# Performance work log

Hardware: AMD Instinct MI355X
Metric: run time of the kernel (lower is better)

The kernel has to match this reference:

```python
import jax, jax.numpy as jnp
import numpy as np

ETA = 1e-5  # option['eta']


def setup_inputs() -> dict:
    key = jax.random.key(0)
    k1, k2, k3, k4 = jax.random.split(key, 4)
    d, N, two_m = 1024, 20000, 512  # num_feature, num_data, 2*m
    At = jax.random.normal(k1, (d, N), dtype=jnp.float32)
    b = jax.random.normal(k2, (N,), dtype=jnp.float32)
    w1_init = jax.random.normal(k3, (d,), dtype=jnp.float32)
    W2_init = jax.random.normal(k4, (two_m, d - 1), dtype=jnp.float32)
    return {"At": At, "b": b, "w1_init": w1_init, "W2_init": W2_init}


def _ftrl_scan(At, b, w1_init, W2_init):
    # Sequential FTRL-style online FM update (task='reg'), faithful to the torch loop.
    def step(carry, xs):
        w1, W2, g_w1, g_W2 = carry
        x, bi = xs                     # x: (d,), bi: scalar
        a = x[:-1]                     # alpha[:-1], (d-1,)
        t = W2 @ a                     # (2m,) == W2.matmul(alpha[:-1])
        scalar = jnp.dot(w1, x) + jnp.dot(t, t)   # w1^T x + t^T t
        sign = 2.0 * (scalar - bi)     # grad of squared loss
        g_w1 = g_w1 + sign * x
        g_W2 = g_W2 + 2.0 * jnp.outer(t, a)       # 2 * (W2 a) a^T
        w1_new = -ETA * g_w1
        W2_new = -ETA * g_W2
        return (w1_new, W2_new, g_w1, g_W2), scalar

    carry0 = (w1_init, W2_init, jnp.zeros_like(w1_init), jnp.zeros_like(W2_init))
    _, preds = jax.lax.scan(step, carry0, (At.T, b))  # scan over num_data
    return preds


def reference(At, b, w1_init, W2_init):
    preds = _ftrl_scan(At, b, w1_init, W2_init)
    return preds, b  # (pred_list, real_list)
```

## Files before the change

### kernel.cpp

```cpp
#include <hip/hip_runtime.h>


#define NN 20000
#define CC 16
#define NCH 1250
#define ETA2 2e-5f
#define XPAD 1028

#define OFF_GRAM 0L
#define OFF_Z    150016L
#define OFF_SCLP 1430016L
#define OFF_ACC  1430080L
#define OFF_TV   1450080L
#define OFF_X0   1470080L

__global__ __launch_bounds__(1024) void k_init(
    const float* __restrict__ At, const float* __restrict__ bvec,
    const float* __restrict__ w1, const float* __restrict__ W2,
    float* __restrict__ out, float* __restrict__ scalp,
    float* __restrict__ x0ws) {
  __shared__ float x0s[1024];
  __shared__ float part[16];
  const int bid = blockIdx.x, t = threadIdx.x;
  const int wid = t >> 6, lane = t & 63;

  if (bid < 32) {
    x0s[t] = (t < 1023) ? At[(long)t * NN] : 0.f;
    __syncthreads();
    const int row = bid * 16 + wid;
    float p = 0.f;
#pragma unroll
    for (int k = 0; k < 16; ++k) {
      const int ci = k * 64 + lane;
      if (ci < 1023) p = fmaf(W2[(long)row * 1023 + ci], x0s[ci], p);
    }
#pragma unroll
    for (int o = 32; o > 0; o >>= 1) p += __shfl_down(p, o);
    if (lane == 0) part[wid] = p * p;
    __syncthreads();
    if (t == 0) {
      float s = 0.f;
#pragma unroll
      for (int k = 0; k < 16; ++k) s += part[k];
      scalp[bid] = s;
    }
  } else if (bid == 32) {
    const float xv = At[(long)t * NN];
    x0ws[t] = xv;
    float p = w1[t] * xv;
#pragma unroll
    for (int o = 32; o > 0; o >>= 1) p += __shfl_down(p, o);
    if (lane == 0) part[wid] = p;
    __syncthreads();
    if (t == 0) {
      float s = 0.f;
#pragma unroll
      for (int k = 0; k < 16; ++k) s += part[k];
      scalp[32] = s;
    }
  } else {
    const int i = (bid - 33) * 1000 + t;
    if (t < 1000) out[NN + i] = bvec[i];
  }
}

#define STAGE_LD(g, dst)                                          \
  {                                                               \
    const int e_ = (g) >> 2, q_ = (g) & 3;                        \
    dst = *(const float4*)(At + (long)e_ * NN + i0 + 4 * q_);     \
  }
#define STAGE_ST(g, src, xl)                                      \
  {                                                               \
    const int e_ = (g) >> 2, q_ = (g) & 3;                        \
    xl[(4 * q_ + 0) * XPAD + e_] = src.x;                         \
    xl[(4 * q_ + 1) * XPAD + e_] = src.y;                         \
    xl[(4 * q_ + 2) * XPAD + e_] = src.z;                         \
    xl[(4 * q_ + 3) * XPAD + e_] = src.w;                         \
  }

struct GramSh {
  __align__(16) float xl[CC * XPAD];
  __align__(16) float x0s[1024];
  float up[64];
  float rs[CC];
  float sc[2];
};
static_assert(sizeof(GramSh) <= 80 * 1024, "LDS too big for 2 blocks/CU");

#define GACC(r, s, RA, RB)                      \
  ac[r][s] = fmaf(RA.x, RB.x, ac[r][s]);        \
  ac[r][s] = fmaf(RA.y, RB.y, ac[r][s]);        \
  ac[r][s] = fmaf(RA.z, RB.z, ac[r][s]);        \
  ac[r][s] = fmaf(RA.w, RB.w, ac[r][s]);

__global__ __launch_bounds__(1024, 4) void k_gram(
    const float* __restrict__ At, const float* __restrict__ bvec,
    const float* __restrict__ x0g, float* __restrict__ gram,
    float* __restrict__ Zr, const float* __restrict__ scalp,
    float* __restrict__ acc) {
  __shared__ GramSh sh;
  const int c = blockIdx.x, t = threadIdx.x;
  const long i0 = (long)c * CC;

  sh.x0s[t] = x0g[t];
  if (t == 0) {
    float T = 0.f;
#pragma unroll
    for (int k = 0; k < 32; ++k) T += scalp[k];
    sh.sc[0] = T;
    sh.sc[1] = scalp[32];
  }

  const bool act = (t < 320);
  const int tile = t >> 5, band = t & 31;
  int a = 0, bb = 0;
  if (act) {
    int r = tile;
    while (r > a) { r -= ++a; }
    bb = r;
  }
  const bool uact = (t >= 320 && t < 384);
  const int uz = t - 320, ub = uz >> 4, ui = uz & 15;
  float4 uac = make_float4(0.f, 0.f, 0.f, 0.f);

  float ac[4][4];
#pragma unroll
  for (int r = 0; r < 4; ++r)
#pragma unroll
    for (int s = 0; s < 4; ++s) ac[r][s] = 0.f;

#define GRAM_PHASE(H)                                                        \
  if (act) {                                                                 \
    _Pragma("unroll") for (int k = 0; k < 4; ++k) {                          \
      const int e0 = (H) * 512 + (band + 32 * k) * 4;                        \
      const float4 A0 = *(const float4*)&sh.xl[(4 * a + 0) * XPAD + e0];     \
      const float4 A1 = *(const float4*)&sh.xl[(4 * a + 1) * XPAD + e0];     \
      const float4 A2 = *(const float4*)&sh.xl[(4 * a + 2) * XPAD + e0];     \
      const float4 A3 = *(const float4*)&sh.xl[(4 * a + 3) * XPAD + e0];     \
      const float4 B0 = *(const float4*)&sh.xl[(4 * bb + 0) * XPAD + e0];    \
      const float4 B1 = *(const float4*)&sh.xl[(4 * bb + 1) * XPAD + e0];    \
      const float4 B2 = *(const float4*)&sh.xl[(4 * bb + 2) * XPAD + e0];    \
      const float4 B3 = *(const float4*)&sh.xl[(4 * bb + 3) * XPAD + e0];    \
      GACC(0, 0, A0, B0) GACC(0, 1, A0, B1) GACC(0, 2, A0, B2)               \
      GACC(0, 3, A0, B3) GACC(1, 0, A1, B0) GACC(1, 1, A1, B1)               \
      GACC(1, 2, A1, B2) GACC(1, 3, A1, B3) GACC(2, 0, A2, B0)               \
      GACC(2, 1, A2, B1) GACC(2, 2, A2, B2) GACC(2, 3, A2, B3)               \
      GACC(3, 0, A3, B0) GACC(3, 1, A3, B1) GACC(3, 2, A3, B2)               \
      GACC(3, 3, A3, B3)                                                     \
    }                                                                        \
  } else if (uact) {                                                         \
    _Pragma("unroll") for (int k = 0; k < 32; ++k) {                         \
      const int e0 = (H) * 512 + ub * 128 + 4 * k;                           \
      const float4 xv = *(const float4*)&sh.xl[ui * XPAD + e0];              \
      const float4 x0 = *(const float4*)&sh.x0s[e0];                         \
      uac.x = fmaf(x0.x, xv.x, uac.x);                                       \
      uac.y = fmaf(x0.y, xv.y, uac.y);                                       \
      uac.z = fmaf(x0.z, xv.z, uac.z);                                       \
      uac.w = fmaf(x0.w, xv.w, uac.w);                                       \
    }                                                                        \
  }

  float4 ha, hb;
  STAGE_LD(t, ha);
  STAGE_LD(1024 + t, hb);
  STAGE_ST(t, ha, sh.xl);
  STAGE_ST(1024 + t, hb, sh.xl);
  __syncthreads();

  STAGE_LD(2048 + t, ha);
  STAGE_LD(3072 + t, hb);

  GRAM_PHASE(0)

  STAGE_ST(2048 + t, ha, sh.xl);
  STAGE_ST(3072 + t, hb, sh.xl);
  __syncthreads();

  GRAM_PHASE(1)

  if (act) {
#pragma unroll
    for (int off = 16; off >= 1; off >>= 1)
#pragma unroll
      for (int r = 0; r < 4; ++r)
#pragma unroll
        for (int s = 0; s < 4; ++s) ac[r][s] += __shfl_xor(ac[r][s], off);
    if (band == 0) {
      float* gp = gram + (long)c * 120;
#pragma unroll
      for (int r = 0; r < 4; ++r) {
        const int row = 4 * a + r;
        const int base = row * (row - 1) / 2;
#pragma unroll
        for (int s = 0; s < 4; ++s) {
          const int col = 4 * bb + s;
          if (col < row) gp[base + col] = ac[r][s];
        }
      }
    }
  }
  if (uact) sh.up[uz] = uac.x + uac.y + uac.z + uac.w;
  __syncthreads();

  if (t < CC) {
    const long gi = i0 + t;
    const float uu = sh.up[t] + sh.up[16 + t] + sh.up[32 + t] + sh.up[48 + t];
    const float qi = sh.xl[t * XPAD + 1023];
    const float q0 = sh.x0s[1023];
    const float al = (gi == 0) ? 1.f : -ETA2 * (uu - q0 * qi);
    const float T0 = sh.sc[0], s0v = sh.sc[1];
    const float bv = bvec[gi];
    float r = 2.f * fmaf(al * al, T0, -bv);
    if (gi == 0) r = 2.f * (s0v + T0 - bv);
    sh.rs[t] = r;
    acc[gi] = r;
  }
  __syncthreads();

  {
    float z = 0.f;
#pragma unroll
    for (int j = 0; j < CC; ++j) z = fmaf(sh.rs[j], sh.xl[j * XPAD + t], z);
    Zr[(long)c * 1024 + t] = z;
  }
}

__global__ __launch_bounds__(1024) void k_scan(float* __restrict__ Z) {
  __shared__ float gsum[32][33];
  const int t = threadIdx.x;
  const int ei = t & 31, ci = t >> 5;
  const int e = blockIdx.x * 32 + ei;
  const int c0 = ci * 40;
  const int c1 = (c0 + 40 < NCH) ? c0 + 40 : NCH;

  float s = 0.f;
  for (int base = c0; base < c1; base += 8) {
    float v[8];
#pragma unroll
    for (int k = 0; k < 8; ++k) {
      const int cc = base + k;
      v[k] = (cc < c1) ? Z[(long)cc * 1024 + e] : 0.f;
    }
#pragma unroll
    for (int k = 0; k < 8; ++k) s += v[k];
  }
  gsum[ci][ei] = s;
  __syncthreads();

  float off = 0.f;
#pragma unroll
  for (int k = 0; k < 31; ++k)
    if (k < ci) off += gsum[k][ei];

  s = off;
  for (int base = c0; base < c1; base += 8) {
    float v[8];
#pragma unroll
    for (int k = 0; k < 8; ++k) {
      const int cc = base + k;
      v[k] = (cc < c1) ? Z[(long)cc * 1024 + e] : 0.f;
    }
#pragma unroll
    for (int k = 0; k < 8; ++k) {
      const int cc = base + k;
      if (cc < c1) Z[(long)cc * 1024 + e] = s;
      s += v[k];
    }
  }
}

struct TermSh {
  __align__(16) float xl[CC * XPAD];
  __align__(16) float Sm[1024];
  float red[512];
  float vvs[CC], wvs[CC];
};
static_assert(sizeof(TermSh) <= 80 * 1024, "LDS too big for 2 blocks/CU");

template <bool LAST>
__global__ __launch_bounds__(1024, 4) void k_term(
    const float* __restrict__ At, const float* __restrict__ bvec,
    const float* __restrict__ gram, const float* __restrict__ S,
    float* __restrict__ Z1, float* __restrict__ acc, float* __restrict__ tvec,
    float* __restrict__ out) {
  __shared__ TermSh sh;
  const int c = blockIdx.x, t = threadIdx.x;
  const long i0 = (long)c * CC;

  sh.Sm[t] = S[(long)c * 1024 + t];
  if (t < CC) sh.vvs[t] = LAST ? tvec[i0 + t] : acc[i0 + t];

  const bool sact = (t < 512);
  const int si = t >> 5, sb = t & 31;
  float p = 0.f;

#define SWEEP_PHASE(H)                                            \
  if (sact) {                                                     \
    _Pragma("unroll") for (int k = 0; k < 4; ++k) {               \
      const int e0 = (H) * 512 + (sb + 32 * k) * 4;               \
      const float4 xv = *(const float4*)&sh.xl[si * XPAD + e0];   \
      const float4 sv = *(const float4*)&sh.Sm[e0];               \
      p = fmaf(xv.x, sv.x, p);                                    \
      p = fmaf(xv.y, sv.y, p);                                    \
      p = fmaf(xv.z, sv.z, p);                                    \
      p = fmaf(xv.w, sv.w, p);                                    \
    }                                                             \
  }

  float4 ha, hb;
  STAGE_LD(t, ha);
  STAGE_LD(1024 + t, hb);
  STAGE_ST(t, ha, sh.xl);
  STAGE_ST(1024 + t, hb, sh.xl);
  __syncthreads();

  STAGE_LD(2048 + t, ha);
  STAGE_LD(3072 + t, hb);

  SWEEP_PHASE(0)

  STAGE_ST(2048 + t, ha, sh.xl);
  STAGE_ST(3072 + t, hb, sh.xl);
  __syncthreads();

  SWEEP_PHASE(1)

  if (sact) sh.red[t] = p;
  __syncthreads();

  if (t < CC) {
    const int i = t;
    float dot = 0.f;
#pragma unroll
    for (int k = 0; k < 32; ++k) dot += sh.red[i * 32 + k];
    const float* grow = gram + (long)c * 120 + i * (i - 1) / 2;
    float g = 0.f;
#pragma unroll 4
    for (int j = 0; j < i; ++j) g = fmaf(grow[j], sh.vvs[j], g);
    const float w = -ETA2 * (dot + g);
    if (LAST) {
      out[i0 + i] = fmaf(0.5f, acc[i0 + i] + w, bvec[i0 + i]);
    } else {
      sh.wvs[i] = w;
      tvec[i0 + i] = w;
      acc[i0 + i] += w;
    }
  }
  if (!LAST) {
    __syncthreads();
    float z = 0.f;
#pragma unroll
    for (int j = 0; j < CC; ++j) z = fmaf(sh.wvs[j], sh.xl[j * XPAD + t], z);
    Z1[(long)c * 1024 + t] = z;
  }
}

extern "C" void kernel_launch(void* const* d_in, const int* in_sizes, int n_in,
                              void* d_out, int out_size, void* d_ws,
                              size_t ws_size, hipStream_t stream) {
  const float* At = (const float*)d_in[0];
  const float* b  = (const float*)d_in[1];
  const float* w1 = (const float*)d_in[2];
  const float* W2 = (const float*)d_in[3];
  float* out = (float*)d_out;
  float* ws = (float*)d_ws;

  float* gram  = ws + OFF_GRAM;
  float* Zsh   = ws + OFF_Z;
  float* scalp = ws + OFF_SCLP;
  float* acc   = ws + OFF_ACC;
  float* tvec  = ws + OFF_TV;
  float* x0ws  = ws + OFF_X0;

  k_init<<<dim3(53), dim3(1024), 0, stream>>>(At, b, w1, W2, out, scalp, x0ws);
  k_gram<<<dim3(NCH), dim3(1024), 0, stream>>>(At, b, x0ws, gram, Zsh, scalp,
                                               acc);
  k_scan<<<dim3(32), dim3(1024), 0, stream>>>(Zsh);
  k_term<false><<<dim3(NCH), dim3(1024), 0, stream>>>(At, b, gram, Zsh, Zsh,
                                                      acc, tvec, out);
  k_scan<<<dim3(32), dim3(1024), 0, stream>>>(Zsh);
  k_term<true><<<dim3(NCH), dim3(1024), 0, stream>>>(At, b, gram, Zsh, Zsh,
                                                     acc, tvec, out);
}
```

Baseline: 228.1 us.

## Halve chunk size and cache chunk-transposed X copy for term passes

Chunk size drops from 16 to 8 columns, so there are 2500 blocks and a smaller triangular Gram (28 entries per chunk) computed one pair per warp-group. The Gram kernel can also write a chunk-major contiguous copy of X into workspace. The term kernels then read it with coalesced float4 loads instead of strided At gathers and LDS transposes, and reduce with wave shuffles. This trades extra workspace traffic (an 80MB copy written once, read twice) against the strided loads, and doubles the length of the scan over chunks.

```diff
diff --git a/kernel.cpp b/kernel.cpp
--- a/kernel.cpp
+++ b/kernel.cpp
@@ -2,17 +2,19 @@
 
 
 #define NN 20000
-#define CC 16
-#define NCH 1250
+#define CC 8
+#define NCH 2500
 #define ETA2 2e-5f
-#define XPAD 1028
+#define XST 1032
 
 #define OFF_GRAM 0L
-#define OFF_Z    150016L
-#define OFF_SCLP 1430016L
-#define OFF_ACC  1430080L
-#define OFF_TV   1450080L
-#define OFF_X0   1470080L
+#define OFF_Z    70016L
+#define OFF_SCLP 2630016L
+#define OFF_ACC  2630080L
+#define OFF_TV   2650112L
+#define OFF_X0   2670144L
+#define OFF_XC   2671168L
+#define WS_NEED_BYTES ((size_t)(OFF_XC + 20480000L) * 4)
 
 __global__ __launch_bounds__(1024) void k_init(
     const float* __restrict__ At, const float* __restrict__ bvec,
@@ -64,40 +66,31 @@
   }
 }
 
-#define STAGE_LD(g, dst)                                          \
-  {                                                               \
-    const int e_ = (g) >> 2, q_ = (g) & 3;                        \
-    dst = *(const float4*)(At + (long)e_ * NN + i0 + 4 * q_);     \
-  }
-#define STAGE_ST(g, src, xl)                                      \
-  {                                                               \
-    const int e_ = (g) >> 2, q_ = (g) & 3;                        \
-    xl[(4 * q_ + 0) * XPAD + e_] = src.x;                         \
-    xl[(4 * q_ + 1) * XPAD + e_] = src.y;                         \
-    xl[(4 * q_ + 2) * XPAD + e_] = src.z;                         \
-    xl[(4 * q_ + 3) * XPAD + e_] = src.w;                         \
+#define STAGE8(g, xl)                                               \
+  {                                                                 \
+    const int e_ = (g) >> 1, q_ = (g) & 1;                          \
+    const float4 v_ =                                               \
+        *(const float4*)(At + (long)e_ * NN + i0 + 4 * q_);         \
+    xl[(4 * q_ + 0) * XST + e_] = v_.x;                             \
+    xl[(4 * q_ + 1) * XST + e_] = v_.y;                             \
+    xl[(4 * q_ + 2) * XST + e_] = v_.z;                             \
+    xl[(4 * q_ + 3) * XST + e_] = v_.w;                             \
   }
 
 struct GramSh {
-  __align__(16) float xl[CC * XPAD];
+  __align__(16) float xl[CC * XST];
   __align__(16) float x0s[1024];
-  float up[64];
+  float usum[CC];
   float rs[CC];
   float sc[2];
 };
-static_assert(sizeof(GramSh) <= 80 * 1024, "LDS too big for 2 blocks/CU");
-
-#define GACC(r, s, RA, RB)                      \
-  ac[r][s] = fmaf(RA.x, RB.x, ac[r][s]);        \
-  ac[r][s] = fmaf(RA.y, RB.y, ac[r][s]);        \
-  ac[r][s] = fmaf(RA.z, RB.z, ac[r][s]);        \
-  ac[r][s] = fmaf(RA.w, RB.w, ac[r][s]);
+static_assert(sizeof(GramSh) <= 64 * 1024, "LDS must stay under 64KB");
 
 __global__ __launch_bounds__(1024, 4) void k_gram(
     const float* __restrict__ At, const float* __restrict__ bvec,
     const float* __restrict__ x0g, float* __restrict__ gram,
     float* __restrict__ Zr, const float* __restrict__ scalp,
-    float* __restrict__ acc) {
+    float* __restrict__ acc, float* __restrict__ Xc, const int writeXc) {
   __shared__ GramSh sh;
   const int c = blockIdx.x, t = threadIdx.x;
   const long i0 = (long)c * CC;
@@ -111,101 +104,52 @@
     sh.sc[1] = scalp[32];
   }
 
-  const bool act = (t < 320);
-  const int tile = t >> 5, band = t & 31;
-  int a = 0, bb = 0;
-  if (act) {
-    int r = tile;
-    while (r > a) { r -= ++a; }
-    bb = r;
-  }
-  const bool uact = (t >= 320 && t < 384);
-  const int uz = t - 320, ub = uz >> 4, ui = uz & 15;
-  float4 uac = make_float4(0.f, 0.f, 0.f, 0.f);
-
-  float ac[4][4];
-#pragma unroll
-  for (int r = 0; r < 4; ++r)
-#pragma unroll
-    for (int s = 0; s < 4; ++s) ac[r][s] = 0.f;
-
-#define GRAM_PHASE(H)                                                        \
-  if (act) {                                                                 \
-    _Pragma("unroll") for (int k = 0; k < 4; ++k) {                          \
-      const int e0 = (H) * 512 + (band + 32 * k) * 4;                        \
-      const float4 A0 = *(const float4*)&sh.xl[(4 * a + 0) * XPAD + e0];     \
-      const float4 A1 = *(const float4*)&sh.xl[(4 * a + 1) * XPAD + e0];     \
-      const float4 A2 = *(const float4*)&sh.xl[(4 * a + 2) * XPAD + e0];     \
-      const float4 A3 = *(const float4*)&sh.xl[(4 * a + 3) * XPAD + e0];     \
-      const float4 B0 = *(const float4*)&sh.xl[(4 * bb + 0) * XPAD + e0];    \
-      const float4 B1 = *(const float4*)&sh.xl[(4 * bb + 1) * XPAD + e0];    \
-      const float4 B2 = *(const float4*)&sh.xl[(4 * bb + 2) * XPAD + e0];    \
-      const float4 B3 = *(const float4*)&sh.xl[(4 * bb + 3) * XPAD + e0];    \
-      GACC(0, 0, A0, B0) GACC(0, 1, A0, B1) GACC(0, 2, A0, B2)               \
-      GACC(0, 3, A0, B3) GACC(1, 0, A1, B0) GACC(1, 1, A1, B1)               \
-      GACC(1, 2, A1, B2) GACC(1, 3, A1, B3) GACC(2, 0, A2, B0)               \
-      GACC(2, 1, A2, B1) GACC(2, 2, A2, B2) GACC(2, 3, A2, B3)               \
-      GACC(3, 0, A3, B0) GACC(3, 1, A3, B1) GACC(3, 2, A3, B2)               \
-      GACC(3, 3, A3, B3)                                                     \
-    }                                                                        \
-  } else if (uact) {                                                         \
-    _Pragma("unroll") for (int k = 0; k < 32; ++k) {                         \
-      const int e0 = (H) * 512 + ub * 128 + 4 * k;                           \
-      const float4 xv = *(const float4*)&sh.xl[ui * XPAD + e0];              \
-      const float4 x0 = *(const float4*)&sh.x0s[e0];                         \
-      uac.x = fmaf(x0.x, xv.x, uac.x);                                       \
-      uac.y = fmaf(x0.y, xv.y, uac.y);                                       \
-      uac.z = fmaf(x0.z, xv.z, uac.z);                                       \
-      uac.w = fmaf(x0.w, xv.w, uac.w);                                       \
-    }                                                                        \
-  }
-
-  float4 ha, hb;
-  STAGE_LD(t, ha);
-  STAGE_LD(1024 + t, hb);
-  STAGE_ST(t, ha, sh.xl);
-  STAGE_ST(1024 + t, hb, sh.xl);
-  __syncthreads();
-
-  STAGE_LD(2048 + t, ha);
-  STAGE_LD(3072 + t, hb);
-
-  GRAM_PHASE(0)
-
-  STAGE_ST(2048 + t, ha, sh.xl);
-  STAGE_ST(3072 + t, hb, sh.xl);
-  __syncthreads();
-
-  GRAM_PHASE(1)
-
-  if (act) {
-#pragma unroll
-    for (int off = 16; off >= 1; off >>= 1)
-#pragma unroll
-      for (int r = 0; r < 4; ++r)
-#pragma unroll
-        for (int s = 0; s < 4; ++s) ac[r][s] += __shfl_xor(ac[r][s], off);
-    if (band == 0) {
-      float* gp = gram + (long)c * 120;
-#pragma unroll
-      for (int r = 0; r < 4; ++r) {
-        const int row = 4 * a + r;
-        const int base = row * (row - 1) / 2;
-#pragma unroll
-        for (int s = 0; s < 4; ++s) {
-          const int col = 4 * bb + s;
-          if (col < row) gp[base + col] = ac[r][s];
-        }
-      }
-    }
-  }
-  if (uact) sh.up[uz] = uac.x + uac.y + uac.z + uac.w;
+  STAGE8(t, sh.xl);
+  STAGE8(1024 + t, sh.xl);
+  __syncthreads();
+
+  if (t < 896) {
+    const int pi = t >> 5, band = t & 31;
+    int i = 1;
+    while ((i + 1) * i / 2 <= pi) ++i;
+    const int j = pi - i * (i - 1) / 2;
+    float p = 0.f;
+#pragma unroll
+    for (int k = 0; k < 8; ++k) {
+      const int ef = (band + 32 * k) * 4;
+      const float4 A = *(const float4*)&sh.xl[i * XST + ef];
+      const float4 B = *(const float4*)&sh.xl[j * XST + ef];
+      p = fmaf(A.x, B.x, p);
+      p = fmaf(A.y, B.y, p);
+      p = fmaf(A.z, B.z, p);
+      p = fmaf(A.w, B.w, p);
+    }
+#pragma unroll
+    for (int off = 16; off >= 1; off >>= 1) p += __shfl_xor(p, off);
+    if (band == 0) gram[(long)c * 28 + pi] = p;
+  } else {
+    const int uz = t - 896, uj = uz >> 4, b16 = uz & 15;
+    float p = 0.f;
+#pragma unroll
+    for (int k = 0; k < 16; ++k) {
+      const int ef = (b16 + 16 * k) * 4;
+      const float4 X = *(const float4*)&sh.xl[uj * XST + ef];
+      const float4 X0 = *(const float4*)&sh.x0s[ef];
+      p = fmaf(X.x, X0.x, p);
+      p = fmaf(X.y, X0.y, p);
+      p = fmaf(X.z, X0.z, p);
+      p = fmaf(X.w, X0.w, p);
+    }
+#pragma unroll
+    for (int off = 8; off >= 1; off >>= 1) p += __shfl_xor(p, off);
+    if (b16 == 0) sh.usum[uj] = p;
+  }
   __syncthreads();
 
   if (t < CC) {
     const long gi = i0 + t;
-    const float uu = sh.up[t] + sh.up[16 + t] + sh.up[32 + t] + sh.up[48 + t];
-    const float qi = sh.xl[t * XPAD + 1023];
+    const float uu = sh.usum[t];
+    const float qi = sh.xl[t * XST + 1023];
     const float q0 = sh.x0s[1023];
     const float al = (gi == 0) ? 1.f : -ETA2 * (uu - q0 * qi);
     const float T0 = sh.sc[0], s0v = sh.sc[1];
@@ -218,10 +162,18 @@
   __syncthreads();
 
   {
+    float x[CC];
+#pragma unroll
+    for (int j = 0; j < CC; ++j) x[j] = sh.xl[j * XST + t];
     float z = 0.f;
 #pragma unroll
-    for (int j = 0; j < CC; ++j) z = fmaf(sh.rs[j], sh.xl[j * XPAD + t], z);
+    for (int j = 0; j < CC; ++j) z = fmaf(sh.rs[j], x[j], z);
     Zr[(long)c * 1024 + t] = z;
+    if (writeXc) {
+      float* dst = Xc + ((long)c * 1024 + t) * CC;
+      *(float4*)dst = make_float4(x[0], x[1], x[2], x[3]);
+      *(float4*)(dst + 4) = make_float4(x[4], x[5], x[6], x[7]);
+    }
   }
 }
 
@@ -230,8 +182,8 @@
   const int t = threadIdx.x;
   const int ei = t & 31, ci = t >> 5;
   const int e = blockIdx.x * 32 + ei;
-  const int c0 = ci * 40;
-  const int c1 = (c0 + 40 < NCH) ? c0 + 40 : NCH;
+  const int c0 = ci * 79;
+  const int c1 = (c0 + 79 < NCH) ? c0 + 79 : NCH;
 
   float s = 0.f;
   for (int base = c0; base < c1; base += 8) {
@@ -269,79 +221,64 @@
   }
 }
 
-struct TermSh {
-  __align__(16) float xl[CC * XPAD];
-  __align__(16) float Sm[1024];
-  float red[512];
-  float vvs[CC], wvs[CC];
-};
-static_assert(sizeof(TermSh) <= 80 * 1024, "LDS too big for 2 blocks/CU");
-
-template <bool LAST>
+template <bool TR, bool LAST>
 __global__ __launch_bounds__(1024, 4) void k_term(
     const float* __restrict__ At, const float* __restrict__ bvec,
     const float* __restrict__ gram, const float* __restrict__ S,
     float* __restrict__ Z1, float* __restrict__ acc, float* __restrict__ tvec,
-    float* __restrict__ out) {
-  __shared__ TermSh sh;
+    float* __restrict__ out, const float* __restrict__ Xc) {
+  __shared__ float red[16][CC];
+  __shared__ float vvs[CC], wvs[CC];
+  __shared__ float xl[TR ? 16 : CC * XST];
   const int c = blockIdx.x, t = threadIdx.x;
+  const int wid = t >> 6, lane = t & 63;
   const long i0 = (long)c * CC;
 
-  sh.Sm[t] = S[(long)c * 1024 + t];
-  if (t < CC) sh.vvs[t] = LAST ? tvec[i0 + t] : acc[i0 + t];
-
-  const bool sact = (t < 512);
-  const int si = t >> 5, sb = t & 31;
-  float p = 0.f;
-
-#define SWEEP_PHASE(H)                                            \
-  if (sact) {                                                     \
-    _Pragma("unroll") for (int k = 0; k < 4; ++k) {               \
-      const int e0 = (H) * 512 + (sb + 32 * k) * 4;               \
-      const float4 xv = *(const float4*)&sh.xl[si * XPAD + e0];   \
-      const float4 sv = *(const float4*)&sh.Sm[e0];               \
-      p = fmaf(xv.x, sv.x, p);                                    \
-      p = fmaf(xv.y, sv.y, p);                                    \
-      p = fmaf(xv.z, sv.z, p);                                    \
-      p = fmaf(xv.w, sv.w, p);                                    \
-    }                                                             \
-  }
-
-  float4 ha, hb;
-  STAGE_LD(t, ha);
-  STAGE_LD(1024 + t, hb);
-  STAGE_ST(t, ha, sh.xl);
-  STAGE_ST(1024 + t, hb, sh.xl);
-  __syncthreads();
-
-  STAGE_LD(2048 + t, ha);
-  STAGE_LD(3072 + t, hb);
-
-  SWEEP_PHASE(0)
-
-  STAGE_ST(2048 + t, ha, sh.xl);
-  STAGE_ST(3072 + t, hb, sh.xl);
-  __syncthreads();
-
-  SWEEP_PHASE(1)
-
-  if (sact) sh.red[t] = p;
+  if (t < CC) vvs[t] = LAST ? tvec[i0 + t] : acc[i0 + t];
+
+  float x[CC];
+  if (TR) {
+    const float* src = Xc + ((long)c * 1024 + t) * CC;
+    const float4 a = *(const float4*)src;
+    const float4 b4 = *(const float4*)(src + 4);
+    x[0] = a.x; x[1] = a.y; x[2] = a.z; x[3] = a.w;
+    x[4] = b4.x; x[5] = b4.y; x[6] = b4.z; x[7] = b4.w;
+  } else {
+    STAGE8(t, xl);
+    STAGE8(1024 + t, xl);
+    __syncthreads();
+#pragma unroll
+    for (int j = 0; j < CC; ++j) x[j] = xl[j * XST + t];
+  }
+
+  const float sv = S[(long)c * 1024 + t];
+  float p[CC];
+#pragma unroll
+  for (int j = 0; j < CC; ++j) p[j] = x[j] * sv;
+#pragma unroll
+  for (int off = 32; off >= 1; off >>= 1)
+#pragma unroll
+    for (int j = 0; j < CC; ++j) p[j] += __shfl_xor(p[j], off);
+  if (lane == 0)
+#pragma unroll
+    for (int j = 0; j < CC; ++j) red[wid][j] = p[j];
   __syncthreads();
 
   if (t < CC) {
     const int i = t;
     float dot = 0.f;
 #pragma unroll
-    for (int k = 0; k < 32; ++k) dot += sh.red[i * 32 + k];
-    const float* grow = gram + (long)c * 120 + i * (i - 1) / 2;
+    for (int k = 0; k < 16; ++k) dot += red[k][i];
+    const float* grow = gram + (long)c * 28 + i * (i - 1) / 2;
     float g = 0.f;
-#pragma unroll 4
-    for (int j = 0; j < i; ++j) g = fmaf(grow[j], sh.vvs[j], g);
+#pragma unroll
+    for (int j = 0; j < CC - 1; ++j)
+      if (j < i) g = fmaf(grow[j], vvs[j], g);
     const float w = -ETA2 * (dot + g);
     if (LAST) {
       out[i0 + i] = fmaf(0.5f, acc[i0 + i] + w, bvec[i0 + i]);
     } else {
-      sh.wvs[i] = w;
+      wvs[i] = w;
       tvec[i0 + i] = w;
       acc[i0 + i] += w;
     }
@@ -350,7 +287,7 @@
     __syncthreads();
     float z = 0.f;
 #pragma unroll
-    for (int j = 0; j < CC; ++j) z = fmaf(sh.wvs[j], sh.xl[j * XPAD + t], z);
+    for (int j = 0; j < CC; ++j) z = fmaf(wvs[j], x[j], z);
     Z1[(long)c * 1024 + t] = z;
   }
 }
@@ -371,14 +308,25 @@
   float* acc   = ws + OFF_ACC;
   float* tvec  = ws + OFF_TV;
   float* x0ws  = ws + OFF_X0;
+  float* Xc    = ws + OFF_XC;
+
+  const int bigws = (ws_size >= WS_NEED_BYTES) ? 1 : 0;
 
   k_init<<<dim3(53), dim3(1024), 0, stream>>>(At, b, w1, W2, out, scalp, x0ws);
   k_gram<<<dim3(NCH), dim3(1024), 0, stream>>>(At, b, x0ws, gram, Zsh, scalp,
-                                               acc);
+                                               acc, Xc, bigws);
   k_scan<<<dim3(32), dim3(1024), 0, stream>>>(Zsh);
-  k_term<false><<<dim3(NCH), dim3(1024), 0, stream>>>(At, b, gram, Zsh, Zsh,
-                                                      acc, tvec, out);
-  k_scan<<<dim3(32), dim3(1024), 0, stream>>>(Zsh);
-  k_term<true><<<dim3(NCH), dim3(1024), 0, stream>>>(At, b, gram, Zsh, Zsh,
-                                                     acc, tvec, out);
-}
+  if (bigws) {
+    k_term<true, false><<<dim3(NCH), dim3(1024), 0, stream>>>(
+        At, b, gram, Zsh, Zsh, acc, tvec, out, Xc);
+    k_scan<<<dim3(32), dim3(1024), 0, stream>>>(Zsh);
+    k_term<true, true><<<dim3(NCH), dim3(1024), 0, stream>>>(
+        At, b, gram, Zsh, Zsh, acc, tvec, out, Xc);
+  } else {
+    k_term<false, false><<<dim3(NCH), dim3(1024), 0, stream>>>(
+        At, b, gram, Zsh, Zsh, acc, tvec, out, Xc);
+    k_scan<<<dim3(32), dim3(1024), 0, stream>>>(Zsh);
+    k_term<false, true><<<dim3(NCH), dim3(1024), 0, stream>>>(
+        At, b, gram, Zsh, Zsh, acc, tvec, out, Xc);
+  }
+}
```

Result: slower. 253.2 us (+11.0%).
